# Kernel tuning notes

Hardware: AMD Instinct MI355X
Metric: run time of the kernel (lower is better)

The kernel has to match this reference:

```python
import jax, jax.numpy as jnp
import numpy as np

H, W, C = 192, 192, 1024

def setup_inputs() -> dict:
    key = jax.random.key(0)
    k1, k2 = jax.random.split(key)
    x = jax.random.normal(k1, (1, H, W, C), dtype=jnp.float32)
    gamma = jax.random.normal(k2, (1,), dtype=jnp.float32)
    return {"x": x, "gamma": gamma}

def reference(x, gamma):
    b, h, w, c = x.shape
    # NOTE: faithful to the TF code: a pure reshape of NHWC into (1, C, H*W),
    # with NO transpose (the original relies on reshape semantics).
    proj = x.reshape(1, c, h * w)                      # query == key^T == value
    energy = jnp.einsum('bcn,bdn->bcd', proj, proj)    # (1, C, C)
    energy_new = jnp.max(energy, axis=-1, keepdims=True) - energy  # sign-flipped
    attention = jax.nn.softmax(energy_new, axis=-1)    # (1, C, C)
    out = jnp.einsum('bcd,bdn->bcn', attention, proj)  # (1, C, H*W)
    out = out.reshape(1, h, w, c)
    return gamma * out + x
```

## Files before the change

kernel.cpp:

```cpp
#include <hip/hip_runtime.h>
#include <cstdint>

#define C_DIM 1024
#define N_DIM 36864

typedef unsigned short ushort_t;
typedef __attribute__((ext_vector_type(8))) short bf16x8;
typedef __attribute__((ext_vector_type(4))) float f32x4;

__device__ __forceinline__ ushort_t f2b(float f) {
    unsigned u = __float_as_uint(f);
    u = (u + 0x7fffu + ((u >> 16) & 1u)) >> 16;
    return (ushort_t)u;
}
__device__ __forceinline__ float b2f(ushort_t b) {
    return __uint_as_float(((unsigned)b) << 16);
}

__device__ __forceinline__ void async16(const void* g, const void* lds) {
    __builtin_amdgcn_global_load_lds(
        (const __attribute__((address_space(1))) unsigned int*)(uintptr_t)g,
        (__attribute__((address_space(3))) unsigned int*)(uint32_t)(uintptr_t)lds,
        16, 0, 0);
}


__global__ __launch_bounds__(256) void k_convert(const float* __restrict__ x,
                                                 ushort_t* __restrict__ ph,
                                                 ushort_t* __restrict__ pl) {
    int i = blockIdx.x * 256 + threadIdx.x;
    float4 v = ((const float4*)x)[i];
    ushort4 h, l;
    h.x = f2b(v.x); l.x = f2b(v.x - b2f(h.x));
    h.y = f2b(v.y); l.y = f2b(v.y - b2f(h.y));
    h.z = f2b(v.z); l.z = f2b(v.z - b2f(h.z));
    h.w = f2b(v.w); l.w = f2b(v.w - b2f(h.w));
    ((ushort4*)ph)[i] = h;
    ((ushort4*)pl)[i] = l;
}

__global__ __launch_bounds__(256) void k_convtrans(const float* __restrict__ x,
                                                   ushort_t* __restrict__ ph,
                                                   ushort_t* __restrict__ pl,
                                                   ushort_t* __restrict__ pht) {
    __shared__ __align__(16) ushort_t th[64][72];
    const int t = threadIdx.x;
    const int i = t >> 2, qd = t & 3;
    const int c0 = blockIdx.y << 6;
    const size_t n0 = (size_t)blockIdx.x << 6;

    const size_t row = (size_t)(c0 + i) * N_DIM + n0 + (qd << 4);
    const float* src = x + row;
    union { ushort_t s[16]; uint4 q[2]; } H, Lo;
#pragma unroll
    for (int u4 = 0; u4 < 4; ++u4) {
        float4 v = ((const float4*)src)[u4];
        ushort_t h0 = f2b(v.x), h1 = f2b(v.y), h2 = f2b(v.z), h3 = f2b(v.w);
        H.s[u4 * 4 + 0] = h0; Lo.s[u4 * 4 + 0] = f2b(v.x - b2f(h0));
        H.s[u4 * 4 + 1] = h1; Lo.s[u4 * 4 + 1] = f2b(v.y - b2f(h1));
        H.s[u4 * 4 + 2] = h2; Lo.s[u4 * 4 + 2] = f2b(v.z - b2f(h2));
        H.s[u4 * 4 + 3] = h3; Lo.s[u4 * 4 + 3] = f2b(v.w - b2f(h3));
    }
    *(uint4*)(ph + row)     = H.q[0];
    *(uint4*)(ph + row + 8) = H.q[1];
    *(uint4*)(pl + row)     = Lo.q[0];
    *(uint4*)(pl + row + 8) = Lo.q[1];
    *(uint4*)&th[i][qd << 4]       = H.q[0];
    *(uint4*)&th[i][(qd << 4) + 8] = H.q[1];
    __syncthreads();

    ushort_t tmp[16];
#pragma unroll
    for (int u = 0; u < 16; ++u) tmp[u] = th[(qd << 4) + u][i];
    ushort_t* dst = pht + (n0 + i) * C_DIM + c0 + (qd << 4);
    *(uint4*)dst       = *(uint4*)tmp;
    *(uint4*)(dst + 8) = *(uint4*)(tmp + 8);
}

__global__ __launch_bounds__(256, 2) void k_egemm(const ushort_t* __restrict__ ph,
                                                  const ushort_t* __restrict__ pl,
                                                  float* __restrict__ g1,
                                                  float* __restrict__ g2,
                                                  int kchunk) {
    __shared__ __align__(16) ushort_t sA [2][128 * 32];
    __shared__ __align__(16) ushort_t sBh[2][128 * 32];
    __shared__ __align__(16) ushort_t sBl[2][128 * 32];

    const int t = threadIdx.x;
    const int w = t >> 6;
    const int L = t & 63;
    const int c0 = blockIdx.x << 7;
    const int d0 = blockIdx.y << 7;
    const int kb = blockIdx.z * kchunk;
    const int lrow = L >> 2;
    const int lcol = (((L & 3) ^ ((L >> 3) & 3)) << 3);

    const ushort_t* gA0 = ph + (size_t)(c0 + (w << 5) + lrow) * N_DIM + kb + lcol;
    const ushort_t* gH0 = ph + (size_t)(d0 + (w << 5) + lrow) * N_DIM + kb + lcol;
    const ushort_t* gL0 = pl + (size_t)(d0 + (w << 5) + lrow) * N_DIM + kb + lcol;
    ushort_t* lA[2] = { sA[0]  + (w << 10), sA[1]  + (w << 10) };
    ushort_t* lH[2] = { sBh[0] + (w << 10), sBh[1] + (w << 10) };
    ushort_t* lL[2] = { sBl[0] + (w << 10), sBl[1] + (w << 10) };

    const int wm = (w >> 1) << 6;
    const int wn = (w & 1) << 6;
    const int lm = L & 15, q = L >> 4;
    const int co = ((q ^ ((lm >> 1) & 3)) << 3);

    f32x4 acc1[4][4], acc2[4][4];
#pragma unroll
    for (int a = 0; a < 4; ++a)
#pragma unroll
        for (int b = 0; b < 4; ++b) { acc1[a][b] = (f32x4)0.0f; acc2[a][b] = (f32x4)0.0f; }

    auto stage = [&](int ti, int b) {
        const ushort_t* ga = gA0 + (ti << 5);
        const ushort_t* gh = gH0 + (ti << 5);
        const ushort_t* gl = gL0 + (ti << 5);
        async16(ga,              lA[b]);
        async16(ga + 16 * N_DIM, lA[b] + 512);
        async16(gh,              lH[b]);
        async16(gh + 16 * N_DIM, lH[b] + 512);
        async16(gl,              lL[b]);
        async16(gl + 16 * N_DIM, lL[b] + 512);
    };

    const int nIter = kchunk >> 5;
    stage(0, 0);

    for (int ti = 0; ti < nIter; ++ti) {
        const int cb = ti & 1;
        if (ti + 1 < nIter) {
            stage(ti + 1, cb ^ 1);
            __builtin_amdgcn_s_waitcnt(0x0F76);
        } else {
            __builtin_amdgcn_s_waitcnt(0x0F70);
        }
        __builtin_amdgcn_s_barrier();

        bf16x8 a[4], bh[4], bl[4];
#pragma unroll
        for (int mt = 0; mt < 4; ++mt)
            a[mt] = *(const bf16x8*)(sA[cb] + ((wm + (mt << 4) + lm) << 5) + co);
#pragma unroll
        for (int nt = 0; nt < 4; ++nt) {
            bh[nt] = *(const bf16x8*)(sBh[cb] + ((wn + (nt << 4) + lm) << 5) + co);
            bl[nt] = *(const bf16x8*)(sBl[cb] + ((wn + (nt << 4) + lm) << 5) + co);
        }
#pragma unroll
        for (int mt = 0; mt < 4; ++mt)
#pragma unroll
            for (int nt = 0; nt < 4; ++nt) {
                acc1[mt][nt] = __builtin_amdgcn_mfma_f32_16x16x32_bf16(a[mt], bh[nt], acc1[mt][nt], 0, 0, 0);
                acc2[mt][nt] = __builtin_amdgcn_mfma_f32_16x16x32_bf16(a[mt], bl[nt], acc2[mt][nt], 0, 0, 0);
            }
        __builtin_amdgcn_s_barrier();
    }

    const size_t zb = (size_t)blockIdx.z << 20;
#pragma unroll
    for (int mt = 0; mt < 4; ++mt)
#pragma unroll
        for (int nt = 0; nt < 4; ++nt)
#pragma unroll
            for (int r = 0; r < 4; ++r) {
                int cg = c0 + wm + (mt << 4) + (q << 2) + r;
                int dg = d0 + wn + (nt << 4) + lm;
                size_t o = zb + ((size_t)cg << 10) + dg;
                g1[o] = acc1[mt][nt][r];
                g2[o] = acc2[mt][nt][r];
            }
}

__global__ __launch_bounds__(256) void k_reduce(const float* __restrict__ g1,
                                                const float* __restrict__ g2,
                                                float* __restrict__ E,
                                                int splitk) {
    __shared__ float ld[64][65];
    const int t = threadIdx.x;
    const int i = t >> 2;
    const int jb = (t & 3) << 4;
    const int c0 = blockIdx.y << 6;
    const int d0 = blockIdx.x << 6;

    float acc[16];
#pragma unroll
    for (int u = 0; u < 16; ++u) acc[u] = 0.0f;

    for (int z = 0; z < splitk; ++z) {
        const size_t zb = (size_t)z << 20;
        const float* p1 = g1 + zb + ((size_t)(c0 + i) << 10) + d0 + jb;
        const float* p2 = g2 + zb + ((size_t)(c0 + i) << 10) + d0 + jb;
        const float* pt = g2 + zb + ((size_t)(d0 + i) << 10) + c0 + jb;
#pragma unroll
        for (int u4 = 0; u4 < 4; ++u4) {
            float4 v1 = ((const float4*)p1)[u4];
            float4 v2 = ((const float4*)p2)[u4];
            acc[u4 * 4 + 0] += v1.x + v2.x;
            acc[u4 * 4 + 1] += v1.y + v2.y;
            acc[u4 * 4 + 2] += v1.z + v2.z;
            acc[u4 * 4 + 3] += v1.w + v2.w;
        }
        __syncthreads();
#pragma unroll
        for (int u4 = 0; u4 < 4; ++u4)
            *(float4*)&ld[i][jb + u4 * 4] = ((const float4*)pt)[u4];
        __syncthreads();
#pragma unroll
        for (int u = 0; u < 16; ++u)
            acc[u] += ld[jb + u][i];
    }

    float* eo = E + ((size_t)(c0 + i) << 10) + d0 + jb;
#pragma unroll
    for (int u4 = 0; u4 < 4; ++u4) {
        float4 v;
        v.x = acc[u4 * 4 + 0]; v.y = acc[u4 * 4 + 1];
        v.z = acc[u4 * 4 + 2]; v.w = acc[u4 * 4 + 3];
        ((float4*)eo)[u4] = v;
    }
}

__global__ __launch_bounds__(256) void k_softmax(const float* __restrict__ E,
                                                 ushort_t* __restrict__ att) {
    const int c = blockIdx.x;
    const int t = threadIdx.x;
    __shared__ float red[4];
    __shared__ float bcast;

    float4 e4 = ((const float4*)E)[((size_t)c << 8) + t];
    float m = fminf(fminf(e4.x, e4.y), fminf(e4.z, e4.w));
#pragma unroll
    for (int off = 32; off > 0; off >>= 1) m = fminf(m, __shfl_down(m, off));
    if ((t & 63) == 0) red[t >> 6] = m;
    __syncthreads();
    if (t == 0) bcast = fminf(fminf(red[0], red[1]), fminf(red[2], red[3]));
    __syncthreads();
    m = bcast;

    float w0 = expf(m - e4.x), w1 = expf(m - e4.y);
    float w2 = expf(m - e4.z), w3 = expf(m - e4.w);
    float s = w0 + w1 + w2 + w3;
#pragma unroll
    for (int off = 32; off > 0; off >>= 1) s += __shfl_down(s, off);
    if ((t & 63) == 0) red[t >> 6] = s;
    __syncthreads();
    if (t == 0) bcast = red[0] + red[1] + red[2] + red[3];
    __syncthreads();
    float inv = 1.0f / bcast;
    ushort4 o;
    o.x = f2b(w0 * inv); o.y = f2b(w1 * inv);
    o.z = f2b(w2 * inv); o.w = f2b(w3 * inv);
    ((ushort4*)att)[((size_t)c << 8) + t] = o;
}

__global__ __launch_bounds__(256) void k_transpose(const ushort_t* __restrict__ ph,
                                                   ushort_t* __restrict__ pht) {
    __shared__ __align__(16) ushort_t tile[64][72];
    const int t = threadIdx.x;
    const int i = t >> 2, qd = t & 3;
    const int c0 = blockIdx.y << 6;
    const size_t n0 = (size_t)blockIdx.x << 6;

    const ushort_t* src = ph + (size_t)(c0 + i) * N_DIM + n0 + (qd << 4);
    uint4 v0 = *(const uint4*)src;
    uint4 v1 = *(const uint4*)(src + 8);
    *(uint4*)&tile[i][qd << 4]       = v0;
    *(uint4*)&tile[i][(qd << 4) + 8] = v1;
    __syncthreads();

    ushort_t tmp[16];
#pragma unroll
    for (int u = 0; u < 16; ++u) tmp[u] = tile[(qd << 4) + u][i];
    ushort_t* dst = pht + (n0 + i) * C_DIM + c0 + (qd << 4);
    *(uint4*)dst       = *(uint4*)tmp;
    *(uint4*)(dst + 8) = *(uint4*)(tmp + 8);
}

__global__ __launch_bounds__(256) void k_ogemm(const ushort_t* __restrict__ att,
                                               const ushort_t* __restrict__ pht,
                                               const float* __restrict__ x,
                                               const float* __restrict__ gamma,
                                               float* __restrict__ out) {
    __shared__ __align__(16) ushort_t sA[128 * 32];
    __shared__ __align__(16) ushort_t sB[128 * 32];

    const int t = threadIdx.x;
    const int w = t >> 6, L = t & 63;
    const int n0 = blockIdx.x << 7;
    const int c0 = blockIdx.y << 7;
    const int srow = L >> 2;
    const int scol = (((L & 3) ^ ((L >> 3) & 3)) << 3);

    const int wm = (w >> 1) << 6, wn = (w & 1) << 6;
    const int lm = L & 15, q = L >> 4;
    const int co = ((q ^ ((lm >> 1) & 3)) << 3);

    f32x4 acc[4][4];
#pragma unroll
    for (int a = 0; a < 4; ++a)
#pragma unroll
        for (int b = 0; b < 4; ++b) acc[a][b] = (f32x4)0.0f;

    for (int k = 0; k < C_DIM; k += 32) {
#pragma unroll
        for (int j = 0; j < 4; ++j) {
            int ch = (w << 2) + j;
            int row = ((ch & 7) << 4) + srow;
            const ushort_t* src = (ch < 8)
                ? att + (size_t)(c0 + row) * C_DIM + k + scol
                : pht + (size_t)(n0 + row) * C_DIM + k + scol;
            ushort_t* base = (ch < 8) ? sA : sB;
            async16(src, base + (((ch & 7) << 4) << 5));
        }
        __syncthreads();

        bf16x8 a[4], b[4];
#pragma unroll
        for (int mt = 0; mt < 4; ++mt)
            a[mt] = *(const bf16x8*)(sA + ((wm + (mt << 4) + lm) << 5) + co);
#pragma unroll
        for (int nt = 0; nt < 4; ++nt)
            b[nt] = *(const bf16x8*)(sB + ((wn + (nt << 4) + lm) << 5) + co);
#pragma unroll
        for (int mt = 0; mt < 4; ++mt)
#pragma unroll
            for (int nt = 0; nt < 4; ++nt)
                acc[mt][nt] = __builtin_amdgcn_mfma_f32_16x16x32_bf16(a[mt], b[nt], acc[mt][nt], 0, 0, 0);
        __syncthreads();
    }

    const float g = gamma[0];
#pragma unroll
    for (int mt = 0; mt < 4; ++mt)
#pragma unroll
        for (int nt = 0; nt < 4; ++nt)
#pragma unroll
            for (int r = 0; r < 4; ++r) {
                int cg = c0 + wm + (mt << 4) + (q << 2) + r;
                int ng = n0 + wn + (nt << 4) + lm;
                size_t o = (size_t)cg * N_DIM + ng;
                out[o] = g * acc[mt][nt][r] + x[o];
            }
}

extern "C" void kernel_launch(void* const* d_in, const int* in_sizes, int n_in,
                              void* d_out, int out_size, void* d_ws, size_t ws_size,
                              hipStream_t stream) {
    const float* x     = (const float*)d_in[0];
    const float* gamma = (const float*)d_in[1];
    float* out = (float*)d_out;
    char* ws = (char*)d_ws;

    const size_t P = 75497472ull, SL = 4194304ull, EB = 4194304ull, AT = 2097152ull;

    int S = 8;
    bool fused = (ws_size >= 3 * P + (size_t)S * 2 * SL + EB + AT);
    if (!fused) {
        if (ws_size < 2 * P + (size_t)S * 2 * SL + EB + AT) S = 4;
        if (ws_size < 2 * P + (size_t)S * 2 * SL + EB + AT) S = 3;
    }
    const int kchunk = N_DIM / S;

    if (fused) {
        ushort_t* ph  = (ushort_t*)(ws);
        ushort_t* pl  = (ushort_t*)(ws + P);
        ushort_t* pht = (ushort_t*)(ws + 2 * P);
        float*    g1  = (float*)   (ws + 3 * P);
        float*    g2  = (float*)   (ws + 3 * P + (size_t)S * SL);
        float*    E   = (float*)   (ws + 3 * P + (size_t)S * 2 * SL);
        ushort_t* att = (ushort_t*)(ws + 3 * P + (size_t)S * 2 * SL + EB);

        k_convtrans<<<dim3(N_DIM / 64, C_DIM / 64), 256, 0, stream>>>(x, ph, pl, pht);
        k_egemm<<<dim3(8, 8, S), 256, 0, stream>>>(ph, pl, g1, g2, kchunk);
        k_reduce<<<dim3(16, 16), 256, 0, stream>>>(g1, g2, E, S);
        k_softmax<<<dim3(C_DIM), 256, 0, stream>>>(E, att);
        k_ogemm<<<dim3(N_DIM / 128, C_DIM / 128), 256, 0, stream>>>(att, pht, x, gamma, out);
    } else {
        ushort_t* ph  = (ushort_t*)(ws);
        ushort_t* pl  = (ushort_t*)(ws + P);
        float*    g1  = (float*)   (ws + 2 * P);
        float*    g2  = (float*)   (ws + 2 * P + (size_t)S * SL);
        float*    E   = (float*)   (ws + 2 * P + (size_t)S * 2 * SL);
        ushort_t* att = (ushort_t*)(ws + 2 * P + (size_t)S * 2 * SL + EB);
        ushort_t* pht = pl;

        k_convert<<<dim3((C_DIM * (size_t)N_DIM / 4) / 256), 256, 0, stream>>>(x, ph, pl);
        k_egemm<<<dim3(8, 8, S), 256, 0, stream>>>(ph, pl, g1, g2, kchunk);
        k_reduce<<<dim3(16, 16), 256, 0, stream>>>(g1, g2, E, S);
        k_softmax<<<dim3(C_DIM), 256, 0, stream>>>(E, att);
        k_transpose<<<dim3(N_DIM / 64, C_DIM / 64), 256, 0, stream>>>(ph, pht);
        k_ogemm<<<dim3(N_DIM / 128, C_DIM / 128), 256, 0, stream>>>(att, pht, x, gamma, out);
    }
}
```

Before: 666.1 us.

## Exploit Gram symmetry: compute upper-triangle tiles only, double-buffer output GEMM

The energy GEMM now runs only on the 36 upper-triangular 128x128 tile pairs of the symmetric Gram matrix instead of all 64. Each block computes the hi*hi plus the two cross terms (hi*lo and lo*hi) explicitly. The reduce kernel mirrors off-diagonal tiles by transposing them through LDS, and split-K grows to 12 to keep the GPU occupied. The output GEMM gains double-buffered async LDS staging. The tradeoff is about 50% more MFMA work per tile, more LDS and lower occupancy in egemm, and a larger split-K partial buffer.

```diff
diff --git a/kernel.cpp b/kernel.cpp
--- a/kernel.cpp
+++ b/kernel.cpp
@@ -82,25 +82,31 @@
                                                   float* __restrict__ g1,
                                                   float* __restrict__ g2,
                                                   int kchunk) {
-    __shared__ __align__(16) ushort_t sA [2][128 * 32];
+    __shared__ __align__(16) ushort_t sAh[2][128 * 32];
+    __shared__ __align__(16) ushort_t sAl[2][128 * 32];
     __shared__ __align__(16) ushort_t sBh[2][128 * 32];
     __shared__ __align__(16) ushort_t sBl[2][128 * 32];
 
     const int t = threadIdx.x;
     const int w = t >> 6;
     const int L = t & 63;
-    const int c0 = blockIdx.x << 7;
-    const int d0 = blockIdx.y << 7;
+
+    int pr = blockIdx.x, pi = 0;
+    while (pr >= 8 - pi) { pr -= 8 - pi; ++pi; }
+    const int c0 = pi << 7;
+    const int d0 = (pi + pr) << 7;
+
     const int kb = blockIdx.z * kchunk;
     const int lrow = L >> 2;
     const int lcol = (((L & 3) ^ ((L >> 3) & 3)) << 3);
 
-    const ushort_t* gA0 = ph + (size_t)(c0 + (w << 5) + lrow) * N_DIM + kb + lcol;
-    const ushort_t* gH0 = ph + (size_t)(d0 + (w << 5) + lrow) * N_DIM + kb + lcol;
-    const ushort_t* gL0 = pl + (size_t)(d0 + (w << 5) + lrow) * N_DIM + kb + lcol;
-    ushort_t* lA[2] = { sA[0]  + (w << 10), sA[1]  + (w << 10) };
-    ushort_t* lH[2] = { sBh[0] + (w << 10), sBh[1] + (w << 10) };
-    ushort_t* lL[2] = { sBl[0] + (w << 10), sBl[1] + (w << 10) };
+    const size_t rA = (size_t)(c0 + (w << 5) + lrow) * N_DIM + kb + lcol;
+    const size_t rB = (size_t)(d0 + (w << 5) + lrow) * N_DIM + kb + lcol;
+    const ushort_t* gAh = ph + rA;
+    const ushort_t* gAl = pl + rA;
+    const ushort_t* gBh = ph + rB;
+    const ushort_t* gBl = pl + rB;
+    const int wb = w << 10;
 
     const int wm = (w >> 1) << 6;
     const int wn = (w & 1) << 6;
@@ -114,15 +120,15 @@
         for (int b = 0; b < 4; ++b) { acc1[a][b] = (f32x4)0.0f; acc2[a][b] = (f32x4)0.0f; }
 
     auto stage = [&](int ti, int b) {
-        const ushort_t* ga = gA0 + (ti << 5);
-        const ushort_t* gh = gH0 + (ti << 5);
-        const ushort_t* gl = gL0 + (ti << 5);
-        async16(ga,              lA[b]);
-        async16(ga + 16 * N_DIM, lA[b] + 512);
-        async16(gh,              lH[b]);
-        async16(gh + 16 * N_DIM, lH[b] + 512);
-        async16(gl,              lL[b]);
-        async16(gl + 16 * N_DIM, lL[b] + 512);
+        const int o = ti << 5;
+        async16(gAh + o,              sAh[b] + wb);
+        async16(gAh + o + 16 * N_DIM, sAh[b] + wb + 512);
+        async16(gAl + o,              sAl[b] + wb);
+        async16(gAl + o + 16 * N_DIM, sAl[b] + wb + 512);
+        async16(gBh + o,              sBh[b] + wb);
+        async16(gBh + o + 16 * N_DIM, sBh[b] + wb + 512);
+        async16(gBl + o,              sBl[b] + wb);
+        async16(gBl + o + 16 * N_DIM, sBl[b] + wb + 512);
     };
 
     const int nIter = kchunk >> 5;
@@ -132,41 +138,46 @@
         const int cb = ti & 1;
         if (ti + 1 < nIter) {
             stage(ti + 1, cb ^ 1);
-            __builtin_amdgcn_s_waitcnt(0x0F76);
+            __builtin_amdgcn_s_waitcnt(0x0F78);
         } else {
             __builtin_amdgcn_s_waitcnt(0x0F70);
         }
         __builtin_amdgcn_s_barrier();
 
-        bf16x8 a[4], bh[4], bl[4];
+        bf16x8 ah[4], al[4], bh[4], bl[4];
+#pragma unroll
+        for (int mt = 0; mt < 4; ++mt) {
+            const int ro = ((wm + (mt << 4) + lm) << 5) + co;
+            ah[mt] = *(const bf16x8*)(sAh[cb] + ro);
+            al[mt] = *(const bf16x8*)(sAl[cb] + ro);
+        }
+#pragma unroll
+        for (int nt = 0; nt < 4; ++nt) {
+            const int ro = ((wn + (nt << 4) + lm) << 5) + co;
+            bh[nt] = *(const bf16x8*)(sBh[cb] + ro);
+            bl[nt] = *(const bf16x8*)(sBl[cb] + ro);
+        }
 #pragma unroll
         for (int mt = 0; mt < 4; ++mt)
-            a[mt] = *(const bf16x8*)(sA[cb] + ((wm + (mt << 4) + lm) << 5) + co);
-#pragma unroll
-        for (int nt = 0; nt < 4; ++nt) {
-            bh[nt] = *(const bf16x8*)(sBh[cb] + ((wn + (nt << 4) + lm) << 5) + co);
-            bl[nt] = *(const bf16x8*)(sBl[cb] + ((wn + (nt << 4) + lm) << 5) + co);
-        }
-#pragma unroll
-        for (int mt = 0; mt < 4; ++mt)
 #pragma unroll
             for (int nt = 0; nt < 4; ++nt) {
-                acc1[mt][nt] = __builtin_amdgcn_mfma_f32_16x16x32_bf16(a[mt], bh[nt], acc1[mt][nt], 0, 0, 0);
-                acc2[mt][nt] = __builtin_amdgcn_mfma_f32_16x16x32_bf16(a[mt], bl[nt], acc2[mt][nt], 0, 0, 0);
+                acc1[mt][nt] = __builtin_amdgcn_mfma_f32_16x16x32_bf16(ah[mt], bh[nt], acc1[mt][nt], 0, 0, 0);
+                acc2[mt][nt] = __builtin_amdgcn_mfma_f32_16x16x32_bf16(ah[mt], bl[nt], acc2[mt][nt], 0, 0, 0);
+                acc2[mt][nt] = __builtin_amdgcn_mfma_f32_16x16x32_bf16(al[mt], bh[nt], acc2[mt][nt], 0, 0, 0);
             }
         __builtin_amdgcn_s_barrier();
     }
 
-    const size_t zb = (size_t)blockIdx.z << 20;
+    const size_t base = ((size_t)blockIdx.z * 36 + blockIdx.x) << 14;
 #pragma unroll
     for (int mt = 0; mt < 4; ++mt)
 #pragma unroll
         for (int nt = 0; nt < 4; ++nt)
 #pragma unroll
             for (int r = 0; r < 4; ++r) {
-                int cg = c0 + wm + (mt << 4) + (q << 2) + r;
-                int dg = d0 + wn + (nt << 4) + lm;
-                size_t o = zb + ((size_t)cg << 10) + dg;
+                int lr = wm + (mt << 4) + (q << 2) + r;
+                int lc = wn + (nt << 4) + lm;
+                size_t o = base + ((size_t)lr << 7) + lc;
                 g1[o] = acc1[mt][nt][r];
                 g2[o] = acc2[mt][nt][r];
             }
@@ -180,18 +191,22 @@
     const int t = threadIdx.x;
     const int i = t >> 2;
     const int jb = (t & 3) << 4;
-    const int c0 = blockIdx.y << 6;
-    const int d0 = blockIdx.x << 6;
+
+    int pr = blockIdx.x, ci = 0;
+    while (pr >= 16 - ci) { pr -= 16 - ci; ++ci; }
+    const int cb = ci, db = ci + pr;
+    const int i8 = cb >> 1, j8 = db >> 1;
+    const int p = i8 * (17 - i8) / 2 + (j8 - i8);
+    const size_t tbase = ((size_t)p << 14) + ((size_t)(cb & 1) << 13) + ((size_t)(db & 1) << 6);
 
     float acc[16];
 #pragma unroll
     for (int u = 0; u < 16; ++u) acc[u] = 0.0f;
 
     for (int z = 0; z < splitk; ++z) {
-        const size_t zb = (size_t)z << 20;
-        const float* p1 = g1 + zb + ((size_t)(c0 + i) << 10) + d0 + jb;
-        const float* p2 = g2 + zb + ((size_t)(c0 + i) << 10) + d0 + jb;
-        const float* pt = g2 + zb + ((size_t)(d0 + i) << 10) + c0 + jb;
+        const size_t zo = (size_t)z * (36 << 14) + tbase + ((size_t)i << 7) + jb;
+        const float* p1 = g1 + zo;
+        const float* p2 = g2 + zo;
 #pragma unroll
         for (int u4 = 0; u4 < 4; ++u4) {
             float4 v1 = ((const float4*)p1)[u4];
@@ -201,17 +216,9 @@
             acc[u4 * 4 + 2] += v1.z + v2.z;
             acc[u4 * 4 + 3] += v1.w + v2.w;
         }
-        __syncthreads();
-#pragma unroll
-        for (int u4 = 0; u4 < 4; ++u4)
-            *(float4*)&ld[i][jb + u4 * 4] = ((const float4*)pt)[u4];
-        __syncthreads();
-#pragma unroll
-        for (int u = 0; u < 16; ++u)
-            acc[u] += ld[jb + u][i];
-    }
-
-    float* eo = E + ((size_t)(c0 + i) << 10) + d0 + jb;
+    }
+
+    float* eo = E + ((size_t)((cb << 6) + i) << 10) + (db << 6) + jb;
 #pragma unroll
     for (int u4 = 0; u4 < 4; ++u4) {
         float4 v;
@@ -219,6 +226,20 @@
         v.z = acc[u4 * 4 + 2]; v.w = acc[u4 * 4 + 3];
         ((float4*)eo)[u4] = v;
     }
+
+    if (cb != db) {
+#pragma unroll
+        for (int u4 = 0; u4 < 4; ++u4)
+            *(float4*)&ld[i][jb + u4 * 4] = *(float4*)&acc[u4 * 4];
+        __syncthreads();
+        float tmp[16];
+#pragma unroll
+        for (int u = 0; u < 16; ++u) tmp[u] = ld[jb + u][i];
+        float* et = E + ((size_t)((db << 6) + i) << 10) + (cb << 6) + jb;
+#pragma unroll
+        for (int u4 = 0; u4 < 4; ++u4)
+            ((float4*)et)[u4] = *(float4*)&tmp[u4 * 4];
+    }
 }
 
 __global__ __launch_bounds__(256) void k_softmax(const float* __restrict__ E,
@@ -282,8 +303,8 @@
                                                const float* __restrict__ x,
                                                const float* __restrict__ gamma,
                                                float* __restrict__ out) {
-    __shared__ __align__(16) ushort_t sA[128 * 32];
-    __shared__ __align__(16) ushort_t sB[128 * 32];
+    __shared__ __align__(16) ushort_t sA[2][128 * 32];
+    __shared__ __align__(16) ushort_t sB[2][128 * 32];
 
     const int t = threadIdx.x;
     const int w = t >> 6, L = t & 63;
@@ -302,32 +323,45 @@
 #pragma unroll
         for (int b = 0; b < 4; ++b) acc[a][b] = (f32x4)0.0f;
 
-    for (int k = 0; k < C_DIM; k += 32) {
+    auto stage = [&](int k0, int b) {
 #pragma unroll
         for (int j = 0; j < 4; ++j) {
             int ch = (w << 2) + j;
             int row = ((ch & 7) << 4) + srow;
             const ushort_t* src = (ch < 8)
-                ? att + (size_t)(c0 + row) * C_DIM + k + scol
-                : pht + (size_t)(n0 + row) * C_DIM + k + scol;
-            ushort_t* base = (ch < 8) ? sA : sB;
+                ? att + (size_t)(c0 + row) * C_DIM + k0 + scol
+                : pht + (size_t)(n0 + row) * C_DIM + k0 + scol;
+            ushort_t* base = (ch < 8) ? sA[b] : sB[b];
             async16(src, base + (((ch & 7) << 4) << 5));
         }
-        __syncthreads();
+    };
+
+    const int nIter = C_DIM / 32;
+    stage(0, 0);
+
+    for (int ti = 0; ti < nIter; ++ti) {
+        const int cb = ti & 1;
+        if (ti + 1 < nIter) {
+            stage((ti + 1) << 5, cb ^ 1);
+            __builtin_amdgcn_s_waitcnt(0x0F74);
+        } else {
+            __builtin_amdgcn_s_waitcnt(0x0F70);
+        }
+        __builtin_amdgcn_s_barrier();
 
         bf16x8 a[4], b[4];
 #pragma unroll
         for (int mt = 0; mt < 4; ++mt)
-            a[mt] = *(const bf16x8*)(sA + ((wm + (mt << 4) + lm) << 5) + co);
+            a[mt] = *(const bf16x8*)(sA[cb] + ((wm + (mt << 4) + lm) << 5) + co);
 #pragma unroll
         for (int nt = 0; nt < 4; ++nt)
-            b[nt] = *(const bf16x8*)(sB + ((wn + (nt << 4) + lm) << 5) + co);
+            b[nt] = *(const bf16x8*)(sB[cb] + ((wn + (nt << 4) + lm) << 5) + co);
 #pragma unroll
         for (int mt = 0; mt < 4; ++mt)
 #pragma unroll
             for (int nt = 0; nt < 4; ++nt)
                 acc[mt][nt] = __builtin_amdgcn_mfma_f32_16x16x32_bf16(a[mt], b[nt], acc[mt][nt], 0, 0, 0);
-        __syncthreads();
+        __builtin_amdgcn_s_barrier();
     }
 
     const float g = gamma[0];
@@ -352,13 +386,24 @@
     float* out = (float*)d_out;
     char* ws = (char*)d_ws;
 
-    const size_t P = 75497472ull, SL = 4194304ull, EB = 4194304ull, AT = 2097152ull;
-
-    int S = 8;
-    bool fused = (ws_size >= 3 * P + (size_t)S * 2 * SL + EB + AT);
-    if (!fused) {
-        if (ws_size < 2 * P + (size_t)S * 2 * SL + EB + AT) S = 4;
-        if (ws_size < 2 * P + (size_t)S * 2 * SL + EB + AT) S = 3;
+    const size_t P  = 75497472ull;
+    const size_t GT = 2359296ull;
+    const size_t EB = 4194304ull, AT = 2097152ull;
+
+    auto need = [&](int s, bool f) {
+        return (size_t)(f ? 3 : 2) * P + (size_t)s * 2 * GT + EB + AT;
+    };
+
+    int S = 12;
+    bool fused = true;
+    if (ws_size < need(12, true)) {
+        if      (ws_size >= need(8, true)) S = 8;
+        else if (ws_size >= need(4, true)) S = 4;
+        else {
+            fused = false; S = 12;
+            if (ws_size < need(12, false)) S = 8;
+            if (ws_size < need(8,  false)) S = 4;
+        }
     }
     const int kchunk = N_DIM / S;
 
@@ -367,27 +412,27 @@
         ushort_t* pl  = (ushort_t*)(ws + P);
         ushort_t* pht = (ushort_t*)(ws + 2 * P);
         float*    g1  = (float*)   (ws + 3 * P);
-        float*    g2  = (float*)   (ws + 3 * P + (size_t)S * SL);
-        float*    E   = (float*)   (ws + 3 * P + (size_t)S * 2 * SL);
-        ushort_t* att = (ushort_t*)(ws + 3 * P + (size_t)S * 2 * SL + EB);
+        float*    g2  = (float*)   (ws + 3 * P + (size_t)S * GT);
+        float*    E   = (float*)   (ws + 3 * P + (size_t)S * 2 * GT);
+        ushort_t* att = (ushort_t*)(ws + 3 * P + (size_t)S * 2 * GT + EB);
 
         k_convtrans<<<dim3(N_DIM / 64, C_DIM / 64), 256, 0, stream>>>(x, ph, pl, pht);
-        k_egemm<<<dim3(8, 8, S), 256, 0, stream>>>(ph, pl, g1, g2, kchunk);
-        k_reduce<<<dim3(16, 16), 256, 0, stream>>>(g1, g2, E, S);
+        k_egemm<<<dim3(36, 1, S), 256, 0, stream>>>(ph, pl, g1, g2, kchunk);
+        k_reduce<<<dim3(136), 256, 0, stream>>>(g1, g2, E, S);
         k_softmax<<<dim3(C_DIM), 256, 0, stream>>>(E, att);
         k_ogemm<<<dim3(N_DIM / 128, C_DIM / 128), 256, 0, stream>>>(att, pht, x, gamma, out);
     } else {
         ushort_t* ph  = (ushort_t*)(ws);
         ushort_t* pl  = (ushort_t*)(ws + P);
         float*    g1  = (float*)   (ws + 2 * P);
-        float*    g2  = (float*)   (ws + 2 * P + (size_t)S * SL);
-        float*    E   = (float*)   (ws + 2 * P + (size_t)S * 2 * SL);
-        ushort_t* att = (ushort_t*)(ws + 2 * P + (size_t)S * 2 * SL + EB);
+        float*    g2  = (float*)   (ws + 2 * P + (size_t)S * GT);
+        float*    E   = (float*)   (ws + 2 * P + (size_t)S * 2 * GT);
+        ushort_t* att = (ushort_t*)(ws + 2 * P + (size_t)S * 2 * GT + EB);
         ushort_t* pht = pl;
 
         k_convert<<<dim3((C_DIM * (size_t)N_DIM / 4) / 256), 256, 0, stream>>>(x, ph, pl);
-        k_egemm<<<dim3(8, 8, S), 256, 0, stream>>>(ph, pl, g1, g2, kchunk);
-        k_reduce<<<dim3(16, 16), 256, 0, stream>>>(g1, g2, E, S);
+        k_egemm<<<dim3(36, 1, S), 256, 0, stream>>>(ph, pl, g1, g2, kchunk);
+        k_reduce<<<dim3(136), 256, 0, stream>>>(g1, g2, E, S);
         k_softmax<<<dim3(C_DIM), 256, 0, stream>>>(E, att);
         k_transpose<<<dim3(N_DIM / 64, C_DIM / 64), 256, 0, stream>>>(ph, pht);
         k_ogemm<<<dim3(N_DIM / 128, C_DIM / 128), 256, 0, stream>>>(att, pht, x, gamma, out);
```

Result: faster. 628.4 us (-5.7%).
